# Kernel optimization log

Hardware: AMD Instinct MI355X
Metric: run time of the kernel (lower is better)

## Reference

```python
import jax, jax.numpy as jnp
import numpy as np

L = 16384   # sequence length
H = 1024    # feature dim
P = 1024    # state dim (ssm_size=2048, conj_sym=True -> P = ssm_size//2)
STEP_RESCALE = 1.0
CLIP_MAX = -1e-4


def setup_inputs() -> dict:
    key = jax.random.key(0)
    ks = jax.random.split(key, 7)
    log_dt_min, log_dt_max = np.log(0.001), np.log(0.1)
    return {
        "input_sequence": jax.random.normal(ks[0], (L, H), jnp.float32),
        # stable eigenvalues: negative real part
        "Lambda_re": -(jnp.abs(jax.random.normal(ks[1], (P,), jnp.float32)) + 1e-3),
        "Lambda_im": jax.random.normal(ks[2], (P,), jnp.float32) * jnp.pi,
        "B": jax.random.normal(ks[3], (P, H, 2), jnp.float32) / np.sqrt(H),
        "C": jax.random.normal(ks[4], (H, P, 2), jnp.float32) / np.sqrt(P),
        "D": jax.random.normal(ks[5], (H,), jnp.float32),
        "log_step": jax.random.uniform(ks[6], (P, 1), jnp.float32,
                                        minval=log_dt_min, maxval=log_dt_max),
    }


def _binop(q_i, q_j):
    # binary operator of the linear recurrence (diagonal A)
    A_i, b_i = q_i
    A_j, b_j = q_j
    return (A_j * A_i, A_j * b_i + b_j)


def reference(input_sequence, Lambda_re, Lambda_im, B, C, D, log_step):
    # clip_eigs=True: clamp real part at -1e-4
    Lambda = jnp.minimum(Lambda_re, CLIP_MAX) + 1j * Lambda_im        # (P,) complex64
    B_tilde = B[..., 0] + 1j * B[..., 1]                              # (P, H)
    C_tilde = C[..., 0] + 1j * C[..., 1]                              # (H, P)
    step = STEP_RESCALE * jnp.exp(log_step[:, 0])                     # (P,)
    # ZOH discretisation
    Lambda_bar = jnp.exp(Lambda * step)                               # (P,)
    B_bar = ((Lambda_bar - 1.0) / Lambda)[:, None] * B_tilde          # (P, H)
    # input projection: (L,H) @ (H,P) -> (L,P) complex
    Bu = input_sequence.astype(B_bar.dtype) @ B_bar.T
    Lam = jnp.broadcast_to(Lambda_bar, Bu.shape)                      # (L, P)
    # parallel (Blelchley-style) associative scan over time
    _, xs = jax.lax.associative_scan(_binop, (Lam, Bu))               # (L, P)
    # output projection; conj_sym=True -> factor 2 on the real part
    ys = 2.0 * jnp.real(xs @ C_tilde.T)                               # (L, H)
    return ys + input_sequence * D
```

## Files before the change

### kernel.cpp

```cpp
#include <hip/hip_runtime.h>
#include <hip/hip_bf16.h>
#include <stdint.h>


#define L_SEQ 16384
#define H_DIM 1024
#define P_DIM 1024
#define NCH   256
#define TCH   64

typedef __bf16 bf16x8 __attribute__((ext_vector_type(8)));
typedef float  floatx4 __attribute__((ext_vector_type(4)));
using bf16 = __hip_bfloat16;

__device__ __forceinline__ void gld_lds16(const void* g, void* l) {
    __builtin_amdgcn_global_load_lds(
        (const __attribute__((address_space(1))) uint32_t*)g,
        (__attribute__((address_space(3))) uint32_t*)l, 16, 0, 0);
}

__device__ __forceinline__ float lo_bf(uint32_t v) { return __uint_as_float(v << 16); }
__device__ __forceinline__ float hi_bf(uint32_t v) { return __uint_as_float(v & 0xffff0000u); }
__device__ __forceinline__ uint32_t pack_bf(float r, float i) {
    bf16 rb = __float2bfloat16(r), ib = __float2bfloat16(i);
    return ((uint32_t)(*(uint16_t*)&ib) << 16) | (uint32_t)(*(uint16_t*)&rb);
}

__device__ __forceinline__ float rd(const void* p, size_t i, int f) {
    return f ? ((const float*)p)[i]
             : __bfloat162float(((const bf16*)p)[i]);
}

__device__ __forceinline__ int detect_f32(const uint16_t* u) {
    __shared__ int cnt;
    if (threadIdx.x == 0) cnt = 0;
    __syncthreads();
    int c = 0;
    #pragma unroll
    for (int i = 0; i < 8; ++i) {
        int e = (u[threadIdx.x * 8 + i] >> 7) & 0xFF;
        c += (e >= 134);
    }
    if (c) atomicAdd(&cnt, c);
    __syncthreads();
    return cnt > 32;
}

__global__ void convert_u(const void* __restrict__ uin, bf16* __restrict__ ub) {
    const int f = detect_f32((const uint16_t*)uin);
    const size_t g = (size_t)blockIdx.x * 256 + threadIdx.x;
    if (f) {
        const float4* s = (const float4*)uin + g * 2;
        float4 a = s[0], b = s[1];
        alignas(16) bf16 t[8] = {
            __float2bfloat16(a.x), __float2bfloat16(a.y),
            __float2bfloat16(a.z), __float2bfloat16(a.w),
            __float2bfloat16(b.x), __float2bfloat16(b.y),
            __float2bfloat16(b.z), __float2bfloat16(b.w)};
        ((uint4*)ub)[g] = *(const uint4*)t;
    } else {
        ((uint4*)ub)[g] = ((const uint4*)uin)[g];
    }
}

__global__ void prep_all(const void* __restrict__ u,
                         const void* __restrict__ Lre, const void* __restrict__ Lim,
                         const void* __restrict__ lstep, const void* __restrict__ B,
                         const void* __restrict__ C, const void* __restrict__ D,
                         bf16* __restrict__ W1t, bf16* __restrict__ W2t,
                         float* __restrict__ d_f,
                         float2* __restrict__ lam, float2* __restrict__ lamT) {
    const int f = detect_f32((const uint16_t*)u);
    const int p = blockIdx.x;
    float lr = fminf(rd(Lre, p, f), -1e-4f);
    float li = rd(Lim, p, f);
    float s  = expf(rd(lstep, p, f));
    float ea = expf(lr * s);
    float lbr = ea * cosf(li * s), lbi = ea * sinf(li * s);
    float dr = lbr - 1.0f, di = lbi;
    float den = lr * lr + li * li;
    float cr = (dr * lr + di * li) / den;
    float ci = (di * lr - dr * li) / den;
    if (threadIdx.x == 0) {
        lam[p] = make_float2(lbr, lbi);
        float tr = lbr, ti = lbi;
        #pragma unroll
        for (int q = 0; q < 6; ++q) {
            float nr = tr * tr - ti * ti, ni = 2.0f * tr * ti;
            tr = nr; ti = ni;
        }
        lamT[p] = make_float2(tr, ti);
        d_f[p] = rd(D, p, f);
    }
    for (int h = threadIdx.x; h < H_DIM; h += blockDim.x) {
        size_t base = ((size_t)p * H_DIM + h) * 2;
        float br = rd(B, base + 0, f);
        float bi = rd(B, base + 1, f);
        W1t[(size_t)(2 * p)     * H_DIM + h] = __float2bfloat16(cr * br - ci * bi);
        W1t[(size_t)(2 * p + 1) * H_DIM + h] = __float2bfloat16(cr * bi + ci * br);
    }
    const int h = blockIdx.x;
    for (int q = threadIdx.x; q < P_DIM; q += blockDim.x) {
        size_t base = ((size_t)h * P_DIM + q) * 2;
        W2t[(size_t)h * (2 * P_DIM) + 2 * q]     = __float2bfloat16( 2.0f * rd(C, base + 0, f));
        W2t[(size_t)h * (2 * P_DIM) + 2 * q + 1] = __float2bfloat16(-2.0f * rd(C, base + 1, f));
    }
}


#define SB0 __builtin_amdgcn_sched_barrier(0)

#define STAGEH(b, t, h) do {                                                  \
    const int k0_ = (t) * 64;                                                 \
    _Pragma("unroll")                                                         \
    for (int q_ = 0; q_ < 2; ++q_) {                                          \
        const int row_ = ((h) & 1) * 128 + q_ * 64 + srow;                    \
        const int g_   = sg ^ (row_ & 7);                                     \
        if ((h) < 2)                                                          \
            gld_lds16(A + (size_t)(bm + row_) * K + k0_ + g_ * 8,             \
                      sA + (b) * 32768 + ((h) & 1) * 16384 + q_ * 8192 + wave * 1024); \
        else                                                                  \
            gld_lds16(Bt + (size_t)(bn + row_) * K + k0_ + g_ * 8,            \
                      sB + (b) * 32768 + ((h) & 1) * 16384 + q_ * 8192 + wave * 1024); \
    } } while (0)

#define LDA(b, mh) do {                                                       \
    _Pragma("unroll")                                                         \
    for (int mi_ = 0; mi_ < 4; ++mi_) {                                       \
        const int row_ = wm + ((mh) * 4 + mi_) * 16 + fr;                     \
        _Pragma("unroll")                                                     \
        for (int ks_ = 0; ks_ < 2; ++ks_) {                                   \
            const int ch_ = (ks_ * 4 + kq) ^ (row_ & 7);                      \
            af[mi_][ks_] = *(const bf16x8*)(sA + (b) * 32768 + row_ * 128 + ch_ * 16); \
        } } } while (0)

#define LDB_TO(dst, b, nh) do {                                               \
    _Pragma("unroll")                                                         \
    for (int ni_ = 0; ni_ < 2; ++ni_) {                                       \
        const int row_ = wn + ((nh) * 2 + ni_) * 16 + fr;                     \
        _Pragma("unroll")                                                     \
        for (int ks_ = 0; ks_ < 2; ++ks_) {                                   \
            const int ch_ = (ks_ * 4 + kq) ^ (row_ & 7);                      \
            dst[ni_][ks_] = *(const bf16x8*)(sB + (b) * 32768 + row_ * 128 + ch_ * 16); \
        } } } while (0)

#define WAIT_DS do {                                                          \
    asm volatile("s_waitcnt lgkmcnt(0)" ::: "memory");                        \
    SB0;                                                                      \
} while (0)

#define MMA(afv, bfv, mh, nh) do {                                            \
    __builtin_amdgcn_s_setprio(1);                                            \
    _Pragma("unroll")                                                         \
    for (int mi_ = 0; mi_ < 4; ++mi_)                                         \
        _Pragma("unroll")                                                     \
        for (int ni_ = 0; ni_ < 2; ++ni_)                                     \
            _Pragma("unroll")                                                 \
            for (int ks_ = 0; ks_ < 2; ++ks_)                                 \
                acc[(mh) * 4 + mi_][(nh) * 2 + ni_] =                         \
                    __builtin_amdgcn_mfma_f32_16x16x32_bf16(                  \
                        afv[mi_][ks_], bfv[ni_][ks_],                         \
                        acc[(mh) * 4 + mi_][(nh) * 2 + ni_], 0, 0, 0);        \
    __builtin_amdgcn_s_setprio(0);                                            \
} while (0)

template <int N, int K, int MODE>
__global__ __launch_bounds__(512, 2) void gemm256(
    const bf16* __restrict__ A, const bf16* __restrict__ Bt,
    bf16* __restrict__ OutBF, float* __restrict__ OutF,
    const bf16* __restrict__ U, const float* __restrict__ Dvec,
    const float2* __restrict__ lam, float2* __restrict__ aggp) {
    constexpr int NXB = N / 256;
    constexpr int KT  = K / 64;
    __shared__ alignas(16) uint8_t sA[2 * 32768];
    __shared__ alignas(16) uint8_t sB[2 * 32768];

    const int tid  = threadIdx.x;
    const int wave = tid >> 6;
    const int lane = tid & 63;
    const int bid  = blockIdx.x;
    const int xr   = bid & 7;
    const int jj   = bid >> 3;
    const int bx   = jj % NXB;
    const int by   = (jj / NXB) * 8 + xr;
    const int bm   = by * 256, bn = bx * 256;
    const int wm   = (wave >> 2) * 128, wn = (wave & 3) * 64;

    floatx4 acc[8][4] = {};

    const int fr   = lane & 15;
    const int kq   = lane >> 4;
    const int srow = tid >> 3;
    const int sg   = tid & 7;

    STAGEH(0, 0, 0); STAGEH(0, 0, 1); STAGEH(0, 0, 2); STAGEH(0, 0, 3);
    STAGEH(1, 1, 0);
    asm volatile("s_waitcnt vmcnt(2)" ::: "memory");
    SB0;
    __builtin_amdgcn_s_barrier();

    bf16x8 af[4][2], b0[2][2], b1[2][2];

    #pragma unroll 2
    for (int t = 0; t < KT; ++t) {
        const int cur = t & 1;
        LDA(cur, 0);
        LDB_TO(b0, cur, 0);
        if (t + 1 < KT) STAGEH(cur ^ 1, t + 1, 1);
        __builtin_amdgcn_s_barrier();
        WAIT_DS;
        MMA(af, b0, 0, 0);
        __builtin_amdgcn_s_barrier();
        LDB_TO(b1, cur, 1);
        if (t + 1 < KT) STAGEH(cur ^ 1, t + 1, 2);
        __builtin_amdgcn_s_barrier();
        WAIT_DS;
        MMA(af, b1, 0, 1);
        __builtin_amdgcn_s_barrier();
        LDA(cur, 1);
        if (t + 1 < KT) STAGEH(cur ^ 1, t + 1, 3);
        __builtin_amdgcn_s_barrier();
        WAIT_DS;
        MMA(af, b1, 1, 1);
        __builtin_amdgcn_s_barrier();
        if (t + 2 < KT) STAGEH(cur, t + 2, 0);
        __builtin_amdgcn_s_barrier();
        MMA(af, b0, 1, 0);
        if (t + 2 < KT) {
            asm volatile("s_waitcnt vmcnt(2)" ::: "memory");
        } else {
            asm volatile("s_waitcnt vmcnt(0)" ::: "memory");
        }
        SB0;
        __builtin_amdgcn_s_barrier();
    }

    const int col0  = bn + wn + fr;
    const int rbase = bm + wm + kq * 4;
    #pragma unroll
    for (int mi = 0; mi < 8; ++mi) {
        #pragma unroll
        for (int rr = 0; rr < 4; ++rr) {
            const int row = rbase + mi * 16 + rr;
            #pragma unroll
            for (int ni = 0; ni < 4; ++ni) {
                const int c = col0 + ni * 16;
                float v = acc[mi][ni][rr];
                if (MODE == 2) {
                    float uu = __bfloat162float(U[(size_t)row * H_DIM + c]);
                    __builtin_nontemporal_store(v + uu * Dvec[c],
                                                &OutF[(size_t)row * N + c]);
                } else {
                    OutBF[(size_t)row * N + c] = __float2bfloat16(v);
                }
            }
        }
    }

    if (MODE == 1) {
        const int par = fr & 1;
        const int cg0 = (bm + wm) >> 6;
        #pragma unroll
        for (int ni = 0; ni < 4; ++ni) {
            const int ql = (wn + ni * 16 + (fr & ~1)) >> 1;
            const float2 lb = lam[(bn >> 1) + ql];
            const float l1r = lb.x, l1i = lb.y;
            const float l2r = l1r * l1r - l1i * l1i, l2i = 2.f * l1r * l1i;
            const float l4r = l2r * l2r - l2i * l2i, l4i = 2.f * l2r * l2i;
            const float l8r = l4r * l4r - l4i * l4i, l8i = 2.f * l4r * l4i;
            const float l12r = l8r * l4r - l8i * l4i;
            const float l12i = l8r * l4i + l8i * l4r;
            #pragma unroll
            for (int h = 0; h < 2; ++h) {
                float wr_, wi_;
                if      (kq == 0) { wr_ = l12r; wi_ = l12i; }
                else if (kq == 1) { wr_ = l8r;  wi_ = l8i;  }
                else if (kq == 2) { wr_ = l4r;  wi_ = l4i;  }
                else              { wr_ = 1.f;  wi_ = 0.f;  }
                float s = 0.f;
                #pragma unroll
                for (int mi2 = 3; mi2 >= 0; --mi2) {
                    #pragma unroll
                    for (int rr = 3; rr >= 0; --rr) {
                        float own  = acc[h * 4 + mi2][ni][rr];
                        float part = __shfl_xor(own, 1);
                        s += wr_ * own + (par ? wi_ : -wi_) * part;
                        float nr = wr_ * l1r - wi_ * l1i;
                        float nI = wr_ * l1i + wi_ * l1r;
                        wr_ = nr; wi_ = nI;
                    }
                    float nr = wr_ * l12r - wi_ * l12i;
                    float nI = wr_ * l12i + wi_ * l12r;
                    wr_ = nr; wi_ = nI;
                }
                s += __shfl_xor(s, 16);
                s += __shfl_xor(s, 32);
                float other = __shfl_xor(s, 1);
                if (kq == 0 && par == 0)
                    aggp[(size_t)(cg0 + h) * P_DIM + (bn >> 1) + ql] =
                        make_float2(s, other);
            }
        }
    }
}

__global__ void scan_phase2p(const float2* __restrict__ agg,
                             const float2* __restrict__ lamT,
                             float2* __restrict__ carry) {
    const int w = threadIdx.x >> 6;
    const int j = threadIdx.x & 63;
    const int p = blockIdx.x * 4 + w;
    const float2 A = lamT[p];
    float b2r = A.x * A.x - A.y * A.y, b2i = 2.f * A.x * A.y;
    float Br = b2r * b2r - b2i * b2i, Bi = 2.f * b2r * b2i;
    float2 a[4];
    #pragma unroll
    for (int k = 0; k < 4; ++k) a[k] = agg[(size_t)(4 * j + k) * P_DIM + p];
    float xr = 0.f, xi = 0.f;
    #pragma unroll
    for (int k = 0; k < 4; ++k) {
        float nr = A.x * xr - A.y * xi + a[k].x;
        float ni = A.x * xi + A.y * xr + a[k].y;
        xr = nr; xi = ni;
    }
    float cr = Br, ci = Bi, vr = xr, vi = xi;
    #pragma unroll
    for (int d = 1; d < 64; d <<= 1) {
        float pvr = __shfl_up(vr, d), pvi = __shfl_up(vi, d);
        float pcr = __shfl_up(cr, d), pci = __shfl_up(ci, d);
        if (j >= d) {
            float nvr = cr * pvr - ci * pvi + vr;
            float nvi = cr * pvi + ci * pvr + vi;
            float ncr = cr * pcr - ci * pci;
            float nci = cr * pci + ci * pcr;
            vr = nvr; vi = nvi; cr = ncr; ci = nci;
        }
    }
    float sr = __shfl_up(vr, 1), si = __shfl_up(vi, 1);
    if (j == 0) { sr = 0.f; si = 0.f; }
    #pragma unroll
    for (int k = 0; k < 4; ++k) {
        carry[(size_t)(4 * j + k) * P_DIM + p] = make_float2(sr, si);
        float nr = A.x * sr - A.y * si + a[k].x;
        float ni = A.x * si + A.y * sr + a[k].y;
        sr = nr; si = ni;
    }
}

__global__ void scan_phase3(uint32_t* __restrict__ BuX,
                            const float2* __restrict__ lam,
                            const float2* __restrict__ carry) {
    const int p = blockIdx.y * 256 + threadIdx.x;
    const int c = blockIdx.x;
    const float2 lb = lam[p];
    const float2 c0 = carry[(size_t)c * P_DIM + p];
    float xr = c0.x, xi = c0.y;
    uint32_t* b = BuX + (size_t)c * TCH * P_DIM + p;
    #pragma unroll 4
    for (int j = 0; j < TCH; ++j) {
        uint32_t v = *b;
        float nr = lb.x * xr - lb.y * xi + lo_bf(v);
        float ni = lb.x * xi + lb.y * xr + hi_bf(v);
        xr = nr; xi = ni;
        *b = pack_bf(xr, xi);
        b += P_DIM;
    }
}

extern "C" void kernel_launch(void* const* d_in, const int* in_sizes, int n_in,
                              void* d_out, int out_size, void* d_ws, size_t ws_size,
                              hipStream_t stream) {
    float* out = (float*)d_out;

    char* w = (char*)d_ws;
    w += 256;
    float2* lam   = (float2*)w;  w += (size_t)P_DIM * 8;
    float2* lamT  = (float2*)w;  w += (size_t)P_DIM * 8;
    float*  d_f   = (float*)w;   w += (size_t)H_DIM * 4;
    float2* agg   = (float2*)w;  w += (size_t)NCH * P_DIM * 8;
    float2* carry = (float2*)w;  w += (size_t)NCH * P_DIM * 8;
    bf16*   W1t   = (bf16*)w;    w += (size_t)2 * P_DIM * H_DIM * 2;
    bf16*   W2t   = (bf16*)w;    w += (size_t)H_DIM * 2 * P_DIM * 2;
    bf16*   ub    = (bf16*)w;    w += (size_t)L_SEQ * H_DIM * 2;
    bf16*   Xbuf  = (bf16*)w;

    convert_u<<<(L_SEQ * H_DIM / 8) / 256, 256, 0, stream>>>(d_in[0], ub);
    prep_all<<<P_DIM, 256, 0, stream>>>(d_in[0], d_in[1], d_in[2], d_in[6],
                                        d_in[3], d_in[4], d_in[5],
                                        W1t, W2t, d_f, lam, lamT);

    gemm256<2 * P_DIM, H_DIM, 1><<<(2 * P_DIM / 256) * (L_SEQ / 256), 512, 0, stream>>>(
        ub, W1t, Xbuf, nullptr, nullptr, nullptr, lam, agg);

    scan_phase2p<<<P_DIM / 4, 256, 0, stream>>>(agg, lamT, carry);
    scan_phase3<<<dim3(NCH, P_DIM / 256), 256, 0, stream>>>(
        (uint32_t*)Xbuf, lam, carry);

    gemm256<H_DIM, 2 * P_DIM, 2><<<(H_DIM / 256) * (L_SEQ / 256), 512, 0, stream>>>(
        Xbuf, W2t, nullptr, out, ub, d_f, nullptr, nullptr);
}
```

Before: 326.6 us.

## Restructure GEMM main loop: full-tile prefetch two ahead, fewer barriers, split A fragments

Changes the GEMM K-loop schedule so each iteration reads all of its A/B fragments from LDS into separate register sets (afL/afH, b0/b1), using partial lgkmcnt waits to overlap LDS reads with MFMAs. The global-to-LDS staging of the next-next tile is issued after a single barrier, in place of being interleaved in quarters across several barriers. The prologue now preloads two full tiles and the vmcnt threshold rises to match. The aim is to cut barrier count and expose more overlap, at the cost of more live registers, which may hurt occupancy at launch_bounds(512,2).

```diff
diff --git a/kernel.cpp b/kernel.cpp
--- a/kernel.cpp
+++ b/kernel.cpp
@@ -124,14 +124,14 @@
                       sB + (b) * 32768 + ((h) & 1) * 16384 + q_ * 8192 + wave * 1024); \
     } } while (0)
 
-#define LDA(b, mh) do {                                                       \
+#define LDA_TO(dst, b, mh) do {                                               \
     _Pragma("unroll")                                                         \
     for (int mi_ = 0; mi_ < 4; ++mi_) {                                       \
         const int row_ = wm + ((mh) * 4 + mi_) * 16 + fr;                     \
         _Pragma("unroll")                                                     \
         for (int ks_ = 0; ks_ < 2; ++ks_) {                                   \
             const int ch_ = (ks_ * 4 + kq) ^ (row_ & 7);                      \
-            af[mi_][ks_] = *(const bf16x8*)(sA + (b) * 32768 + row_ * 128 + ch_ * 16); \
+            dst[mi_][ks_] = *(const bf16x8*)(sA + (b) * 32768 + row_ * 128 + ch_ * 16); \
         } } } while (0)
 
 #define LDB_TO(dst, b, nh) do {                                               \
@@ -143,11 +143,6 @@
             const int ch_ = (ks_ * 4 + kq) ^ (row_ & 7);                      \
             dst[ni_][ks_] = *(const bf16x8*)(sB + (b) * 32768 + row_ * 128 + ch_ * 16); \
         } } } while (0)
-
-#define WAIT_DS do {                                                          \
-    asm volatile("s_waitcnt lgkmcnt(0)" ::: "memory");                        \
-    SB0;                                                                      \
-} while (0)
 
 #define MMA(afv, bfv, mh, nh) do {                                            \
     __builtin_amdgcn_s_setprio(1);                                            \
@@ -194,40 +189,37 @@
     const int sg   = tid & 7;
 
     STAGEH(0, 0, 0); STAGEH(0, 0, 1); STAGEH(0, 0, 2); STAGEH(0, 0, 3);
-    STAGEH(1, 1, 0);
-    asm volatile("s_waitcnt vmcnt(2)" ::: "memory");
+    STAGEH(1, 1, 0); STAGEH(1, 1, 1); STAGEH(1, 1, 2); STAGEH(1, 1, 3);
+    asm volatile("s_waitcnt vmcnt(8)" ::: "memory");
     SB0;
     __builtin_amdgcn_s_barrier();
 
-    bf16x8 af[4][2], b0[2][2], b1[2][2];
+    bf16x8 afL[4][2], afH[4][2], b0[2][2], b1[2][2];
 
     #pragma unroll 2
     for (int t = 0; t < KT; ++t) {
         const int cur = t & 1;
-        LDA(cur, 0);
-        LDB_TO(b0, cur, 0);
-        if (t + 1 < KT) STAGEH(cur ^ 1, t + 1, 1);
+        LDA_TO(afL, cur, 0); SB0;
+        LDB_TO(b0, cur, 0);  SB0;
+        LDB_TO(b1, cur, 1);  SB0;
+        asm volatile("s_waitcnt lgkmcnt(4)" ::: "memory");
+        SB0;
+        MMA(afL, b0, 0, 0);
+        LDA_TO(afH, cur, 1); SB0;
+        asm volatile("s_waitcnt lgkmcnt(8)" ::: "memory");
+        SB0;
+        MMA(afL, b1, 0, 1);
+        asm volatile("s_waitcnt lgkmcnt(0)" ::: "memory");
+        SB0;
         __builtin_amdgcn_s_barrier();
-        WAIT_DS;
-        MMA(af, b0, 0, 0);
-        __builtin_amdgcn_s_barrier();
-        LDB_TO(b1, cur, 1);
-        if (t + 1 < KT) STAGEH(cur ^ 1, t + 1, 2);
-        __builtin_amdgcn_s_barrier();
-        WAIT_DS;
-        MMA(af, b1, 0, 1);
-        __builtin_amdgcn_s_barrier();
-        LDA(cur, 1);
-        if (t + 1 < KT) STAGEH(cur ^ 1, t + 1, 3);
-        __builtin_amdgcn_s_barrier();
-        WAIT_DS;
-        MMA(af, b1, 1, 1);
-        __builtin_amdgcn_s_barrier();
-        if (t + 2 < KT) STAGEH(cur, t + 2, 0);
-        __builtin_amdgcn_s_barrier();
-        MMA(af, b0, 1, 0);
+        if (t + 2 < KT) { STAGEH(cur, t + 2, 0); STAGEH(cur, t + 2, 2); }
+        SB0;
+        MMA(afH, b1, 1, 1);
+        if (t + 2 < KT) { STAGEH(cur, t + 2, 1); STAGEH(cur, t + 2, 3); }
+        SB0;
+        MMA(afH, b0, 1, 0);
         if (t + 2 < KT) {
-            asm volatile("s_waitcnt vmcnt(2)" ::: "memory");
+            asm volatile("s_waitcnt vmcnt(8)" ::: "memory");
         } else {
             asm volatile("s_waitcnt vmcnt(0)" ::: "memory");
         }
```

Result: slower. 391.5 us (+19.9%).
